# Kernel tuning notes

Measured on AMD Instinct MI355X. Metric: run time of the kernel, lower is better.

The kernel has to match this reference:

```python
import jax, jax.numpy as jnp
import numpy as np

N_NODES = 50000
N_EDGES = 1600000
IN_F = 512
OUT_F = 256


def setup_inputs() -> dict:
    key = jax.random.key(0)
    k1, k2, k3, k4, k5 = jax.random.split(key, 5)
    features = jax.random.normal(k1, (N_NODES, IN_F), dtype=jnp.float32)
    # xavier_uniform init for weight [in_features, out_features]
    limit = np.sqrt(6.0 / (IN_F + OUT_F)).astype(np.float32)
    weight = jax.random.uniform(k2, (IN_F, OUT_F), dtype=jnp.float32,
                                minval=-limit, maxval=limit)
    # COO sparse adjacency (normalized edge weights in [0,1))
    edge_vals = jax.random.uniform(k3, (N_EDGES,), dtype=jnp.float32)
    edge_rows = jax.random.randint(k4, (N_EDGES,), 0, N_NODES, dtype=jnp.int32)
    edge_cols = jax.random.randint(k5, (N_EDGES,), 0, N_NODES, dtype=jnp.int32)
    return {"features": features, "weight": weight, "edge_vals": edge_vals,
            "edge_rows": edge_rows, "edge_cols": edge_cols}


def reference(features, weight, edge_vals, edge_rows, edge_cols):
    # dropout p=0.0 / eval mode -> identity
    support = features @ weight                      # [N, out_f] dense GEMM
    # torch.spmm(adj, support): out[r] += val * support[c] for each edge (r, c)
    gathered = support[edge_cols] * edge_vals[:, None]   # [E, out_f]
    output = jax.ops.segment_sum(gathered, edge_rows, num_segments=N_NODES)
    return jax.nn.relu(output)
```

## Files before the change

kernel.cpp:

```cpp
#include <hip/hip_runtime.h>

#define N_NODES 50000
#define N_EDGES 1600000
#define IN_F    512
#define OUT_F   256

#define BROWS   128
#define NBINS   ((N_NODES + BROWS - 1) / BROWS)
#define BATCH   2048
#define NBATCHES ((N_EDGES + BATCH - 1) / BATCH)

typedef __attribute__((ext_vector_type(8))) short bf16x8;
typedef __attribute__((ext_vector_type(4))) float f32x4;

__device__ __forceinline__ short bf16rne(float f) {
    unsigned u = __builtin_bit_cast(unsigned, f);
    u += 0x7fffu + ((u >> 16) & 1u);
    return (short)(u >> 16);
}

__device__ __forceinline__ float b2f(unsigned short h) {
    unsigned u = (unsigned)h << 16;
    return __builtin_bit_cast(float, u);
}

__global__ __launch_bounds__(256) void wt_kernel(const float* __restrict__ W,
                                                 short* __restrict__ Wt) {
    int idx = blockIdx.x * 256 + threadIdx.x;
    if (idx < IN_F * OUT_F) {
        int n = idx >> 9;
        int k = idx & 511;
        Wt[idx] = bf16rne(W[(size_t)k * OUT_F + n]);
    }
}

#define ASTRIDE 40
#define BSTRIDE 40

__global__ __launch_bounds__(512) void gemm_mfma_kernel(const float* __restrict__ A,
                                                        const short* __restrict__ Wt,
                                                        unsigned short* __restrict__ Cb) {
    __shared__ short As[128 * ASTRIDE];
    __shared__ short Bs[256 * BSTRIDE];

    const int tid  = threadIdx.x;
    const int wave = tid >> 6;
    const int lane = tid & 63;
    const int m0   = blockIdx.x * 128;
    const int wrow = (wave >> 2) * 64;
    const int wcol = (wave & 3) * 64;

    const int quad = lane >> 4;
    const int l16  = lane & 15;

    const int ar = tid >> 2;
    const int aq = tid & 3;

    const int bn = tid >> 1;
    const int bh = tid & 1;

    f32x4 zero4 = {0.f, 0.f, 0.f, 0.f};
    f32x4 acc[4][4];
#pragma unroll
    for (int i = 0; i < 4; ++i)
#pragma unroll
        for (int j = 0; j < 4; ++j) acc[i][j] = zero4;

    for (int k0 = 0; k0 < IN_F; k0 += 32) {
        {
            const int gm = m0 + ar;
            float4 v0 = make_float4(0.f, 0.f, 0.f, 0.f);
            float4 v1 = v0;
            if (gm < N_NODES) {
                const float* p = A + (size_t)gm * IN_F + k0 + aq * 8;
                v0 = *(const float4*)p;
                v1 = *(const float4*)(p + 4);
            }
            bf16x8 b;
            b[0] = bf16rne(v0.x); b[1] = bf16rne(v0.y);
            b[2] = bf16rne(v0.z); b[3] = bf16rne(v0.w);
            b[4] = bf16rne(v1.x); b[5] = bf16rne(v1.y);
            b[6] = bf16rne(v1.z); b[7] = bf16rne(v1.w);
            *(bf16x8*)&As[ar * ASTRIDE + aq * 8] = b;
        }
        {
            const short* src = Wt + (size_t)bn * IN_F + k0 + bh * 16;
            bf16x8 w0 = *(const bf16x8*)(src + 0);
            bf16x8 w1 = *(const bf16x8*)(src + 8);
            short* dst = &Bs[bn * BSTRIDE + bh * 16];
            *(bf16x8*)(dst + 0) = w0;
            *(bf16x8*)(dst + 8) = w1;
        }
        __syncthreads();

        bf16x8 af[4], bf[4];
#pragma unroll
        for (int mt = 0; mt < 4; ++mt)
            af[mt] = *(const bf16x8*)&As[(wrow + mt * 16 + l16) * ASTRIDE + quad * 8];
#pragma unroll
        for (int nt = 0; nt < 4; ++nt)
            bf[nt] = *(const bf16x8*)&Bs[(wcol + nt * 16 + l16) * BSTRIDE + quad * 8];

#pragma unroll
        for (int mt = 0; mt < 4; ++mt)
#pragma unroll
            for (int nt = 0; nt < 4; ++nt)
                acc[mt][nt] = __builtin_amdgcn_mfma_f32_16x16x32_bf16(
                    af[mt], bf[nt], acc[mt][nt], 0, 0, 0);
        __syncthreads();
    }

#pragma unroll
    for (int mt = 0; mt < 4; ++mt) {
        const int rbase = m0 + wrow + mt * 16 + quad * 4;
#pragma unroll
        for (int i = 0; i < 4; ++i) {
            const int row = rbase + i;
            if (row < N_NODES) {
#pragma unroll
                for (int nt = 0; nt < 4; ++nt)
                    Cb[(size_t)row * OUT_F + wcol + nt * 16 + l16] =
                        (unsigned short)bf16rne(acc[mt][nt][i]);
            }
        }
    }
}

__global__ __launch_bounds__(256) void zero_bins_kernel(int* __restrict__ binCounts) {
    int i = blockIdx.x * 256 + threadIdx.x;
    if (i < NBINS) binCounts[i] = 0;
}

__global__ __launch_bounds__(256) void histA_kernel(const int* __restrict__ rows,
                                                    int* __restrict__ binCounts) {
    __shared__ int lh[NBINS];
    const int tid = threadIdx.x;
    for (int i = tid; i < NBINS; i += 256) lh[i] = 0;
    __syncthreads();
    for (int i = blockIdx.x * 256 + tid; i < N_EDGES; i += gridDim.x * 256)
        atomicAdd(&lh[rows[i] >> 7], 1);
    __syncthreads();
    for (int i = tid; i < NBINS; i += 256)
        if (lh[i]) atomicAdd(&binCounts[i], lh[i]);
}

__global__ __launch_bounds__(256) void scanA_kernel(const int* __restrict__ binCounts,
                                                    int* __restrict__ binStart,
                                                    int* __restrict__ gcursor) {
    __shared__ int stmp[256];
    const int tid = threadIdx.x;
    const int i0 = 2 * tid, i1 = 2 * tid + 1;
    const int a0 = (i0 < NBINS) ? binCounts[i0] : 0;
    const int a1 = (i1 < NBINS) ? binCounts[i1] : 0;
    const int pair = a0 + a1;
    stmp[tid] = pair;
    for (int off = 1; off < 256; off <<= 1) {
        __syncthreads();
        int t = (tid >= off) ? stmp[tid - off] : 0;
        __syncthreads();
        stmp[tid] += t;
    }
    __syncthreads();
    const int pexcl = stmp[tid] - pair;
    if (i0 < NBINS) { binStart[i0] = pexcl;      gcursor[i0] = pexcl; }
    if (i1 < NBINS) { binStart[i1] = pexcl + a0; gcursor[i1] = pexcl + a0; }
}

__global__ __launch_bounds__(256) void fillA_kernel(const int* __restrict__ rows,
                                                    const int* __restrict__ cols,
                                                    const float* __restrict__ vals,
                                                    int* __restrict__ gcursor,
                                                    int2* __restrict__ binned) {
    __shared__ int lhist[NBINS];
    __shared__ int lexcl[NBINS];
    __shared__ int gbase[NBINS];
    __shared__ int stmp[256];
    __shared__ int2 lstage[BATCH];
    __shared__ unsigned short sbucket[BATCH];

    const int tid   = threadIdx.x;
    const int start = blockIdx.x * BATCH;
    const int count = min(BATCH, N_EDGES - start);

    for (int i = tid; i < NBINS; i += 256) lhist[i] = 0;
    __syncthreads();

    int myrow[8], myrank[8];
#pragma unroll
    for (int j = 0; j < 8; ++j) {
        const int s = j * 256 + tid;
        if (s < count) {
            const int r = rows[start + s];
            myrow[j]  = r;
            myrank[j] = atomicAdd(&lhist[r >> 7], 1);
        }
    }
    __syncthreads();

    {
        const int i0 = 2 * tid, i1 = 2 * tid + 1;
        const int a0 = (i0 < NBINS) ? lhist[i0] : 0;
        const int a1 = (i1 < NBINS) ? lhist[i1] : 0;
        const int pair = a0 + a1;
        stmp[tid] = pair;
        for (int off = 1; off < 256; off <<= 1) {
            __syncthreads();
            int t = (tid >= off) ? stmp[tid - off] : 0;
            __syncthreads();
            stmp[tid] += t;
        }
        __syncthreads();
        const int pexcl = stmp[tid] - pair;
        if (i0 < NBINS) {
            lexcl[i0] = pexcl;
            gbase[i0] = a0 ? atomicAdd(&gcursor[i0], a0) : 0;
        }
        if (i1 < NBINS) {
            lexcl[i1] = pexcl + a0;
            gbase[i1] = a1 ? atomicAdd(&gcursor[i1], a1) : 0;
        }
    }
    __syncthreads();

#pragma unroll
    for (int j = 0; j < 8; ++j) {
        const int s = j * 256 + tid;
        if (s < count) {
            const int r   = myrow[j];
            const int b   = r >> 7;
            const int pos = lexcl[b] + myrank[j];
            lstage[pos]  = make_int2(((r & 127) << 16) | cols[start + s],
                                     __float_as_int(vals[start + s]));
            sbucket[pos] = (unsigned short)b;
        }
    }
    __syncthreads();

#pragma unroll
    for (int j = 0; j < 8; ++j) {
        const int s = j * 256 + tid;
        if (s < count) {
            const int b = sbucket[s];
            binned[gbase[b] + (s - lexcl[b])] = lstage[s];
        }
    }
}

__global__ __launch_bounds__(256) void sortB_kernel(const int2* __restrict__ binned,
                                                    const int* __restrict__ binStart,
                                                    const int* __restrict__ binCounts,
                                                    int* __restrict__ excl,
                                                    unsigned int* __restrict__ ecv) {
    __shared__ int lhist[BROWS];
    __shared__ int lcur[BROWS];

    const int tid  = threadIdx.x;
    const int b    = blockIdx.x;
    const int base = binStart[b];
    const int cnt  = binCounts[b];

    if (tid < BROWS) lhist[tid] = 0;
    __syncthreads();

    for (int i = tid; i < cnt; i += 256)
        atomicAdd(&lhist[binned[base + i].x >> 16], 1);
    __syncthreads();

    if (tid < BROWS) lcur[tid] = lhist[tid];
    for (int off = 1; off < BROWS; off <<= 1) {
        __syncthreads();
        int t = (tid >= off && tid < BROWS) ? lcur[tid - off] : 0;
        __syncthreads();
        if (tid < BROWS) lcur[tid] += t;
    }
    __syncthreads();
    if (tid < BROWS) {
        const int pexcl = lcur[tid] - lhist[tid];
        const int row   = b * BROWS + tid;
        lcur[tid] = pexcl;
        if (row < N_NODES) excl[row] = base + pexcl;
    }
    __syncthreads();

    for (int i = tid; i < cnt; i += 256) {
        const int2 e  = binned[base + i];
        const int rl  = e.x >> 16;
        const int col = e.x & 0xFFFF;
        const int rank = atomicAdd(&lcur[rl], 1);
        ecv[base + rank] = ((unsigned int)col << 16) |
                           (unsigned short)bf16rne(__int_as_float(e.y));
    }
}

__global__ __launch_bounds__(256) void gather_kernel(const ushort4* __restrict__ support,
                                                     const int* __restrict__ excl,
                                                     const unsigned int* __restrict__ ecv,
                                                     float4* __restrict__ out,
                                                     int row0) {
    const int tid  = threadIdx.x;
    const int row  = row0 + blockIdx.x * 4 + (tid >> 6);
    const int lane = tid & 63;
    if (row >= N_NODES) return;

    const int start = excl[row];
    const int end   = (row + 1 < N_NODES) ? excl[row + 1] : N_EDGES;

    float4 acc = make_float4(0.f, 0.f, 0.f, 0.f);
    int e = start;
    const int end4 = start + ((end - start) & ~3);
    for (; e < end4; e += 4) {
        const unsigned int p0 = ecv[e];
        const unsigned int p1 = ecv[e + 1];
        const unsigned int p2 = ecv[e + 2];
        const unsigned int p3 = ecv[e + 3];
        const ushort4 s0 = support[(size_t)(p0 >> 16) * 64 + lane];
        const ushort4 s1 = support[(size_t)(p1 >> 16) * 64 + lane];
        const ushort4 s2 = support[(size_t)(p2 >> 16) * 64 + lane];
        const ushort4 s3 = support[(size_t)(p3 >> 16) * 64 + lane];
        const float v0 = b2f((unsigned short)(p0 & 0xFFFF));
        const float v1 = b2f((unsigned short)(p1 & 0xFFFF));
        const float v2 = b2f((unsigned short)(p2 & 0xFFFF));
        const float v3 = b2f((unsigned short)(p3 & 0xFFFF));
        acc.x += v0 * b2f(s0.x); acc.y += v0 * b2f(s0.y);
        acc.z += v0 * b2f(s0.z); acc.w += v0 * b2f(s0.w);
        acc.x += v1 * b2f(s1.x); acc.y += v1 * b2f(s1.y);
        acc.z += v1 * b2f(s1.z); acc.w += v1 * b2f(s1.w);
        acc.x += v2 * b2f(s2.x); acc.y += v2 * b2f(s2.y);
        acc.z += v2 * b2f(s2.z); acc.w += v2 * b2f(s2.w);
        acc.x += v3 * b2f(s3.x); acc.y += v3 * b2f(s3.y);
        acc.z += v3 * b2f(s3.z); acc.w += v3 * b2f(s3.w);
    }
    for (; e < end; ++e) {
        const unsigned int p0 = ecv[e];
        const ushort4 s0 = support[(size_t)(p0 >> 16) * 64 + lane];
        const float v0 = b2f((unsigned short)(p0 & 0xFFFF));
        acc.x += v0 * b2f(s0.x); acc.y += v0 * b2f(s0.y);
        acc.z += v0 * b2f(s0.z); acc.w += v0 * b2f(s0.w);
    }

    acc.x = fmaxf(acc.x, 0.f);
    acc.y = fmaxf(acc.y, 0.f);
    acc.z = fmaxf(acc.z, 0.f);
    acc.w = fmaxf(acc.w, 0.f);
    out[(size_t)row * 64 + lane] = acc;
}

extern "C" void kernel_launch(void* const* d_in, const int* in_sizes, int n_in,
                              void* d_out, int out_size, void* d_ws, size_t ws_size,
                              hipStream_t stream) {
    const float* features  = (const float*)d_in[0];
    const float* weight    = (const float*)d_in[1];
    const float* edge_vals = (const float*)d_in[2];
    const int*   edge_rows = (const int*)d_in[3];
    const int*   edge_cols = (const int*)d_in[4];
    float* out = (float*)d_out;

    unsigned short* support_bf = (unsigned short*)d_ws;
    int2*  binned    = (int2*)(support_bf + (size_t)N_NODES * OUT_F);
    unsigned int* ecv = (unsigned int*)(binned + N_EDGES);
    int*   excl      = (int*)(ecv + N_EDGES);
    int*   binCounts = excl + N_NODES;
    int*   binStart  = binCounts + 512;
    int*   gcursor   = binStart + 512;
    short* Wt        = (short*)(gcursor + 512);

    wt_kernel<<<(IN_F * OUT_F + 255) / 256, 256, 0, stream>>>(weight, Wt);

    gemm_mfma_kernel<<<(N_NODES + 127) / 128, 512, 0, stream>>>(features, Wt, support_bf);

    zero_bins_kernel<<<2, 256, 0, stream>>>(binCounts);
    histA_kernel<<<256, 256, 0, stream>>>(edge_rows, binCounts);
    scanA_kernel<<<1, 256, 0, stream>>>(binCounts, binStart, gcursor);
    fillA_kernel<<<NBATCHES, 256, 0, stream>>>(edge_rows, edge_cols, edge_vals,
                                               gcursor, binned);
    sortB_kernel<<<NBINS, 256, 0, stream>>>(binned, binStart, binCounts, excl, ecv);

    gather_kernel<<<25000 / 4, 256, 0, stream>>>(
        (const ushort4*)support_bf, excl, ecv, (float4*)out, 0);
    gather_kernel<<<25000 / 4, 256, 0, stream>>>(
        (const ushort4*)support_bf, excl, ecv, (float4*)out, 25000);
}
```

Before: 373.0 us.

## Replace two-level binned sort with direct per-row counting sort via global atomics

Replaces the two-pass bucketed CSR build (per-bin histogram, shared-memory staged fill, per-bin local sort) with a flat counting sort: per-row global atomic histogram, single-block scan, and atomic-cursor scatter directly into the final packed edge array. This removes the intermediate binned buffer and two kernels, cutting memory traffic and launches. The trade-off is many contended global atomics on 50k counters, uncoalesced scattered writes, and a serial single-block scan. Within-row edge order becomes nondeterministic, which changes float summation order.

Measured after the change: 591.9 us. 1.59x slower.

```diff
diff --git a/kernel.cpp b/kernel.cpp
--- a/kernel.cpp
+++ b/kernel.cpp
@@ -4,11 +4,6 @@
 #define N_EDGES 1600000
 #define IN_F    512
 #define OUT_F   256
-
-#define BROWS   128
-#define NBINS   ((N_NODES + BROWS - 1) / BROWS)
-#define BATCH   2048
-#define NBATCHES ((N_EDGES + BATCH - 1) / BATCH)
 
 typedef __attribute__((ext_vector_type(8))) short bf16x8;
 typedef __attribute__((ext_vector_type(4))) float f32x4;
@@ -126,169 +121,63 @@
     }
 }
 
-__global__ __launch_bounds__(256) void zero_bins_kernel(int* __restrict__ binCounts) {
+__global__ __launch_bounds__(256) void zero_counts_kernel(int* __restrict__ rowCount) {
     int i = blockIdx.x * 256 + threadIdx.x;
-    if (i < NBINS) binCounts[i] = 0;
-}
-
-__global__ __launch_bounds__(256) void histA_kernel(const int* __restrict__ rows,
-                                                    int* __restrict__ binCounts) {
-    __shared__ int lh[NBINS];
-    const int tid = threadIdx.x;
-    for (int i = tid; i < NBINS; i += 256) lh[i] = 0;
+    if (i < N_NODES) rowCount[i] = 0;
+}
+
+__global__ __launch_bounds__(256) void hist_kernel(const int* __restrict__ rows,
+                                                   int* __restrict__ rowCount) {
+    int i = blockIdx.x * 256 + threadIdx.x;
+    if (i < N_EDGES) atomicAdd(&rowCount[rows[i]], 1);
+}
+
+#define SCAN_T 1024
+#define CHUNK  ((N_NODES + SCAN_T - 1) / SCAN_T)
+
+__global__ __launch_bounds__(SCAN_T) void scan_kernel(const int* __restrict__ rowCount,
+                                                      int* __restrict__ excl,
+                                                      int* __restrict__ cursor) {
+    __shared__ int part[SCAN_T];
+    const int t = threadIdx.x;
+    const int base = t * CHUNK;
+
+    int s = 0;
+    for (int j = 0; j < CHUNK; ++j) {
+        const int i = base + j;
+        if (i < N_NODES) s += rowCount[i];
+    }
+    part[t] = s;
+    for (int off = 1; off < SCAN_T; off <<= 1) {
+        __syncthreads();
+        int v = (t >= off) ? part[t - off] : 0;
+        __syncthreads();
+        part[t] += v;
+    }
     __syncthreads();
-    for (int i = blockIdx.x * 256 + tid; i < N_EDGES; i += gridDim.x * 256)
-        atomicAdd(&lh[rows[i] >> 7], 1);
-    __syncthreads();
-    for (int i = tid; i < NBINS; i += 256)
-        if (lh[i]) atomicAdd(&binCounts[i], lh[i]);
-}
-
-__global__ __launch_bounds__(256) void scanA_kernel(const int* __restrict__ binCounts,
-                                                    int* __restrict__ binStart,
-                                                    int* __restrict__ gcursor) {
-    __shared__ int stmp[256];
-    const int tid = threadIdx.x;
-    const int i0 = 2 * tid, i1 = 2 * tid + 1;
-    const int a0 = (i0 < NBINS) ? binCounts[i0] : 0;
-    const int a1 = (i1 < NBINS) ? binCounts[i1] : 0;
-    const int pair = a0 + a1;
-    stmp[tid] = pair;
-    for (int off = 1; off < 256; off <<= 1) {
-        __syncthreads();
-        int t = (tid >= off) ? stmp[tid - off] : 0;
-        __syncthreads();
-        stmp[tid] += t;
-    }
-    __syncthreads();
-    const int pexcl = stmp[tid] - pair;
-    if (i0 < NBINS) { binStart[i0] = pexcl;      gcursor[i0] = pexcl; }
-    if (i1 < NBINS) { binStart[i1] = pexcl + a0; gcursor[i1] = pexcl + a0; }
-}
-
-__global__ __launch_bounds__(256) void fillA_kernel(const int* __restrict__ rows,
-                                                    const int* __restrict__ cols,
-                                                    const float* __restrict__ vals,
-                                                    int* __restrict__ gcursor,
-                                                    int2* __restrict__ binned) {
-    __shared__ int lhist[NBINS];
-    __shared__ int lexcl[NBINS];
-    __shared__ int gbase[NBINS];
-    __shared__ int stmp[256];
-    __shared__ int2 lstage[BATCH];
-    __shared__ unsigned short sbucket[BATCH];
-
-    const int tid   = threadIdx.x;
-    const int start = blockIdx.x * BATCH;
-    const int count = min(BATCH, N_EDGES - start);
-
-    for (int i = tid; i < NBINS; i += 256) lhist[i] = 0;
-    __syncthreads();
-
-    int myrow[8], myrank[8];
-#pragma unroll
-    for (int j = 0; j < 8; ++j) {
-        const int s = j * 256 + tid;
-        if (s < count) {
-            const int r = rows[start + s];
-            myrow[j]  = r;
-            myrank[j] = atomicAdd(&lhist[r >> 7], 1);
-        }
-    }
-    __syncthreads();
-
-    {
-        const int i0 = 2 * tid, i1 = 2 * tid + 1;
-        const int a0 = (i0 < NBINS) ? lhist[i0] : 0;
-        const int a1 = (i1 < NBINS) ? lhist[i1] : 0;
-        const int pair = a0 + a1;
-        stmp[tid] = pair;
-        for (int off = 1; off < 256; off <<= 1) {
-            __syncthreads();
-            int t = (tid >= off) ? stmp[tid - off] : 0;
-            __syncthreads();
-            stmp[tid] += t;
-        }
-        __syncthreads();
-        const int pexcl = stmp[tid] - pair;
-        if (i0 < NBINS) {
-            lexcl[i0] = pexcl;
-            gbase[i0] = a0 ? atomicAdd(&gcursor[i0], a0) : 0;
-        }
-        if (i1 < NBINS) {
-            lexcl[i1] = pexcl + a0;
-            gbase[i1] = a1 ? atomicAdd(&gcursor[i1], a1) : 0;
-        }
-    }
-    __syncthreads();
-
-#pragma unroll
-    for (int j = 0; j < 8; ++j) {
-        const int s = j * 256 + tid;
-        if (s < count) {
-            const int r   = myrow[j];
-            const int b   = r >> 7;
-            const int pos = lexcl[b] + myrank[j];
-            lstage[pos]  = make_int2(((r & 127) << 16) | cols[start + s],
-                                     __float_as_int(vals[start + s]));
-            sbucket[pos] = (unsigned short)b;
-        }
-    }
-    __syncthreads();
-
-#pragma unroll
-    for (int j = 0; j < 8; ++j) {
-        const int s = j * 256 + tid;
-        if (s < count) {
-            const int b = sbucket[s];
-            binned[gbase[b] + (s - lexcl[b])] = lstage[s];
-        }
-    }
-}
-
-__global__ __launch_bounds__(256) void sortB_kernel(const int2* __restrict__ binned,
-                                                    const int* __restrict__ binStart,
-                                                    const int* __restrict__ binCounts,
-                                                    int* __restrict__ excl,
-                                                    unsigned int* __restrict__ ecv) {
-    __shared__ int lhist[BROWS];
-    __shared__ int lcur[BROWS];
-
-    const int tid  = threadIdx.x;
-    const int b    = blockIdx.x;
-    const int base = binStart[b];
-    const int cnt  = binCounts[b];
-
-    if (tid < BROWS) lhist[tid] = 0;
-    __syncthreads();
-
-    for (int i = tid; i < cnt; i += 256)
-        atomicAdd(&lhist[binned[base + i].x >> 16], 1);
-    __syncthreads();
-
-    if (tid < BROWS) lcur[tid] = lhist[tid];
-    for (int off = 1; off < BROWS; off <<= 1) {
-        __syncthreads();
-        int t = (tid >= off && tid < BROWS) ? lcur[tid - off] : 0;
-        __syncthreads();
-        if (tid < BROWS) lcur[tid] += t;
-    }
-    __syncthreads();
-    if (tid < BROWS) {
-        const int pexcl = lcur[tid] - lhist[tid];
-        const int row   = b * BROWS + tid;
-        lcur[tid] = pexcl;
-        if (row < N_NODES) excl[row] = base + pexcl;
-    }
-    __syncthreads();
-
-    for (int i = tid; i < cnt; i += 256) {
-        const int2 e  = binned[base + i];
-        const int rl  = e.x >> 16;
-        const int col = e.x & 0xFFFF;
-        const int rank = atomicAdd(&lcur[rl], 1);
-        ecv[base + rank] = ((unsigned int)col << 16) |
-                           (unsigned short)bf16rne(__int_as_float(e.y));
+
+    int run = (t > 0) ? part[t - 1] : 0;
+    for (int j = 0; j < CHUNK; ++j) {
+        const int i = base + j;
+        if (i < N_NODES) {
+            excl[i]   = run;
+            cursor[i] = run;
+            run += rowCount[i];
+        }
+    }
+}
+
+__global__ __launch_bounds__(256) void scatter_kernel(const int* __restrict__ rows,
+                                                      const int* __restrict__ cols,
+                                                      const float* __restrict__ vals,
+                                                      int* __restrict__ cursor,
+                                                      unsigned int* __restrict__ ecv) {
+    int i = blockIdx.x * 256 + threadIdx.x;
+    if (i < N_EDGES) {
+        const int r   = rows[i];
+        const int pos = atomicAdd(&cursor[r], 1);
+        ecv[pos] = ((unsigned int)cols[i] << 16) |
+                   (unsigned short)bf16rne(vals[i]);
     }
 }
 
@@ -356,24 +245,21 @@
     float* out = (float*)d_out;
 
     unsigned short* support_bf = (unsigned short*)d_ws;
-    int2*  binned    = (int2*)(support_bf + (size_t)N_NODES * OUT_F);
-    unsigned int* ecv = (unsigned int*)(binned + N_EDGES);
+    unsigned int* ecv = (unsigned int*)(support_bf + (size_t)N_NODES * OUT_F);
     int*   excl      = (int*)(ecv + N_EDGES);
-    int*   binCounts = excl + N_NODES;
-    int*   binStart  = binCounts + 512;
-    int*   gcursor   = binStart + 512;
-    short* Wt        = (short*)(gcursor + 512);
+    int*   cursor    = excl + N_NODES;
+    int*   rowCount  = cursor + N_NODES;
+    short* Wt        = (short*)(rowCount + N_NODES);
 
     wt_kernel<<<(IN_F * OUT_F + 255) / 256, 256, 0, stream>>>(weight, Wt);
 
     gemm_mfma_kernel<<<(N_NODES + 127) / 128, 512, 0, stream>>>(features, Wt, support_bf);
 
-    zero_bins_kernel<<<2, 256, 0, stream>>>(binCounts);
-    histA_kernel<<<256, 256, 0, stream>>>(edge_rows, binCounts);
-    scanA_kernel<<<1, 256, 0, stream>>>(binCounts, binStart, gcursor);
-    fillA_kernel<<<NBATCHES, 256, 0, stream>>>(edge_rows, edge_cols, edge_vals,
-                                               gcursor, binned);
-    sortB_kernel<<<NBINS, 256, 0, stream>>>(binned, binStart, binCounts, excl, ecv);
+    zero_counts_kernel<<<(N_NODES + 255) / 256, 256, 0, stream>>>(rowCount);
+    hist_kernel<<<(N_EDGES + 255) / 256, 256, 0, stream>>>(edge_rows, rowCount);
+    scan_kernel<<<1, SCAN_T, 0, stream>>>(rowCount, excl, cursor);
+    scatter_kernel<<<(N_EDGES + 255) / 256, 256, 0, stream>>>(edge_rows, edge_cols,
+                                                              edge_vals, cursor, ecv);
 
     gather_kernel<<<25000 / 4, 256, 0, stream>>>(
         (const ushort4*)support_bf, excl, ecv, (float4*)out, 0);
```
